# Optimization experiments

Hardware: AMD Instinct MI355X
Metric: run time of the kernel (lower is better)

The kernel has to match this reference:

```python
import jax, jax.numpy as jnp
import numpy as np

DIM = 512
HEADS = 8
DIM_HEAD = 64
INNER = HEADS * DIM_HEAD          # 512
GROUPS = 8                        # offset_groups
OFF_D = INNER // GROUPS           # 64
DS = 4                            # downsample_factor
KS = 6                            # offset_kernel_size
OFF_SCALE = 4.0                   # offset_scale (defaults to downsample_factor)
SCALE = DIM_HEAD ** -0.5


def conv1d(x, w, b=None, stride=1, padding=0, groups=1):
    # x: (B, Cin, N), w: (Cout, Cin//groups, K)
    out = jax.lax.conv_general_dilated(
        x, w, (stride,), [(padding, padding)],
        dimension_numbers=('NCH', 'OIH', 'NCH'), feature_group_count=groups)
    if b is not None:
        out = out + b[None, :, None]
    return out


def grid_sample_1d(feats, grid):
    # Faithful to F.grid_sample(mode='bilinear', padding_mode='zeros', align_corners=False)
    # applied along a length-N axis (the 2D workaround's width dim is size 1 -> identity).
    # feats: (B, C, N), grid: (B, M) normalized coords.
    N = feats.shape[-1]
    pos = ((grid + 1.0) * N - 1.0) * 0.5          # unnormalize, align_corners=False
    x0 = jnp.floor(pos)
    w1 = (pos - x0)[:, None, :]                    # fractional weight, (B,1,M)

    def gather(idx):
        valid = ((idx >= 0) & (idx < N))[:, None, :]
        idxc = jnp.clip(idx, 0, N - 1).astype(jnp.int32)
        g = jnp.take_along_axis(feats, idxc[:, None, :], axis=2)  # (B,C,M)
        return g * valid

    return gather(x0) * (1.0 - w1) + gather(x0 + 1.0) * w1


def setup_inputs() -> dict:
    key = jax.random.key(0)
    ks = jax.random.split(key, 10)
    n = 4096
    x = jax.random.normal(ks[0], (1, n, DIM), dtype=jnp.float32)
    prev_x = jax.random.normal(ks[1], (1, n, DIM), dtype=jnp.float32)

    def w(k, shape, fan_in):
        return jax.random.normal(k, shape, dtype=jnp.float32) * (fan_in ** -0.5)

    Wq = w(ks[2], (INNER, 2 * DIM // GROUPS, 1), 2 * DIM // GROUPS)   # grouped 1x1
    Wk = w(ks[3], (INNER, DIM // GROUPS, 1), DIM // GROUPS)
    Wv = w(ks[4], (INNER, DIM // GROUPS, 1), DIM // GROUPS)
    Wo = w(ks[5], (DIM, INNER, 1), INNER)
    bo = jnp.zeros((DIM,), dtype=jnp.float32)
    Woff_dw = w(ks[6], (OFF_D, 1, KS), KS)                             # depthwise
    boff_dw = jnp.zeros((OFF_D,), dtype=jnp.float32)
    Woff_p = w(ks[7], (1, OFF_D, 1), OFF_D)                            # to 1 channel
    return {"x": x, "prev_x": prev_x, "Wq": Wq, "Wk": Wk, "Wv": Wv,
            "Wo": Wo, "bo": bo, "Woff_dw": Woff_dw, "boff_dw": boff_dw,
            "Woff_p": Woff_p}


def reference(x, prev_x, Wq, Wk, Wv, Wo, bo, Woff_dw, boff_dw, Woff_p):
    b = x.shape[0]                    # must be 1 (module's einsum relies on broadcast)
    x_t = jnp.swapaxes(x, 1, 2)       # (b, dim, n)
    px_t = jnp.swapaxes(prev_x, 1, 2)
    n = x_t.shape[-1]

    cq = jnp.concatenate([px_t, x_t], axis=1)          # (b, 2*dim, n)
    q = conv1d(cq, Wq, groups=GROUPS)                  # (b, inner, n)

    # offset network on grouped queries
    gq = q.reshape(b * GROUPS, OFF_D, n)
    h = conv1d(gq, Woff_dw, boff_dw, stride=DS, padding=(KS - DS) // 2, groups=OFF_D)
    h = jax.nn.gelu(h, approximate=False)
    off = conv1d(h, Woff_p)[:, 0, :]                   # (b*g, m)
    off = jnp.tanh(off) * OFF_SCALE
    m = off.shape[-1]                                  # n // DS

    vgrid = jnp.arange(m, dtype=off.dtype) + off       # (b*g, m)
    vgrid = 2.0 * vgrid / max(m - 1, 1) - 1.0          # normalize_grid
    vgrid = jnp.tile(vgrid, (2, 1))                    # (2*b*g, m)

    kv_in = jnp.concatenate([px_t, x_t], axis=0)       # (2b, dim, n)
    gkv = kv_in.reshape(2 * b * GROUPS, OFF_D, n)
    kv = grid_sample_1d(gkv, vgrid)                    # (2bg, off_d, m)
    kv = kv.reshape(2 * b, INNER, m)

    k = conv1d(kv, Wk, groups=GROUPS)                  # (2b, inner, m)
    v = conv1d(kv, Wv, groups=GROUPS)

    qh = (q * SCALE).reshape(b, HEADS, DIM_HEAD, n).transpose(0, 1, 3, 2)   # (b,h,n,d)
    kh = k.reshape(2 * b, HEADS, DIM_HEAD, m).transpose(0, 1, 3, 2)         # (2b,h,m,d)
    vh = v.reshape(2 * b, HEADS, DIM_HEAD, m).transpose(0, 1, 3, 2)

    qh = jnp.broadcast_to(qh, (2 * b,) + qh.shape[1:])  # explicit torch-einsum broadcast
    sim = jnp.einsum('bhid,bhjd->bhij', qh, kh)         # (2b,h,n,m)
    attn = jax.nn.softmax(sim, axis=-1)
    out = jnp.einsum('bhij,bhjd->bhid', attn, vh)       # (2b,h,n,d)

    out = out.transpose(0, 1, 3, 2).reshape(2 * b, INNER, n)
    out = conv1d(out, Wo, bo)                           # (2b, dim, n)
    out = jnp.swapaxes(out, 1, 2)                       # (2b, n, dim)
    out = out.reshape(2, b, n, DIM)
    return out.mean(axis=0)                             # (b, n, dim) -- avg prev/cur streams
```

## Files before the change

### kernel.cpp

```cpp
#include <hip/hip_runtime.h>
#include <math.h>

#define DIMC 512
#define NG 8
#define QSCALE 0.18033688011112042f
#define MSHIFT 7.2134752044448170f

typedef _Float16 half8 __attribute__((ext_vector_type(8)));
typedef __fp16 fp16x2 __attribute__((ext_vector_type(2)));
typedef float f32x4 __attribute__((ext_vector_type(4)));

__device__ __forceinline__ half8 frag_f32(const float* p) {
    float4 a = *(const float4*)p;
    float4 b = *(const float4*)(p + 4);
    union { fp16x2 h2[4]; half8 h8; } u;
    u.h2[0] = __builtin_amdgcn_cvt_pkrtz(a.x, a.y);
    u.h2[1] = __builtin_amdgcn_cvt_pkrtz(a.z, a.w);
    u.h2[2] = __builtin_amdgcn_cvt_pkrtz(b.x, b.y);
    u.h2[3] = __builtin_amdgcn_cvt_pkrtz(b.z, b.w);
    return u.h8;
}

__global__ __launch_bounds__(256, 2) void k_front(
    const float* __restrict__ x, const float* __restrict__ px,
    const float* __restrict__ Wq, const float* __restrict__ Wk,
    const float* __restrict__ Wv, const float* __restrict__ Wo,
    const float* __restrict__ Wdw, const float* __restrict__ bdw,
    const float* __restrict__ Wp, _Float16* __restrict__ qh,
    _Float16* __restrict__ kt16, _Float16* __restrict__ vt16,
    _Float16* __restrict__ Woh, int n, int m)
{
    __shared__ float Os[64*69];
    __shared__ float hl[2][64];
    __shared__ float part[16][16];
    __shared__ int   x0s[16];
    __shared__ float w1s[16];
    __shared__ _Float16 kvs[2][16*72];
    int g  = blockIdx.x & 7;
    int jt = blockIdx.x >> 3;
    int P0 = jt*64, j0 = jt*16;
    int t  = threadIdx.x;
    int lane = t & 63, w = t >> 6;
    int l15 = lane & 15, quad = lane >> 4;
    const float* SRC = (g < 4) ? px : x;
    int cbase = (g & 3) * 128;

    if (blockIdx.x < 128) {
        int idx = blockIdx.x*2048 + t*8;
        float4 a = *(const float4*)&Wo[idx];
        float4 b = *(const float4*)&Wo[idx+4];
        union { fp16x2 h2[4]; uint4 v; } pk;
        pk.h2[0] = __builtin_amdgcn_cvt_pkrtz(a.x, a.y);
        pk.h2[1] = __builtin_amdgcn_cvt_pkrtz(a.z, a.w);
        pk.h2[2] = __builtin_amdgcn_cvt_pkrtz(b.x, b.y);
        pk.h2[3] = __builtin_amdgcn_cvt_pkrtz(b.z, b.w);
        *(uint4*)&Woh[idx] = pk.v;
    }

    if (t < 128) {
        int side = t >> 6, c = t & 63;
        int p = P0 + (side ? 64 : -1);
        float hsum = 0.f;
        if (p >= 0 && p < n) {
            const float* xr = &SRC[(size_t)p*DIMC + cbase];
            const float* wr = &Wq[(size_t)(g*64 + c)*128];
#pragma unroll 8
            for (int k = 0; k < 32; ++k) {
                float4 xv = *(const float4*)&xr[k*4];
                float4 wv = *(const float4*)&wr[k*4];
                hsum += xv.x*wv.x + xv.y*wv.y + xv.z*wv.z + xv.w*wv.w;
            }
        }
        hl[side][c] = hsum;
    }

    half8 af[4];
#pragma unroll
    for (int ks = 0; ks < 4; ++ks)
        af[ks] = frag_f32(&SRC[(size_t)(P0 + w*16 + l15)*DIMC + cbase + ks*32 + quad*8]);
    f32x4 acc[4];
#pragma unroll
    for (int nt = 0; nt < 4; ++nt) acc[nt] = (f32x4){0.f,0.f,0.f,0.f};
#pragma unroll
    for (int ks = 0; ks < 4; ++ks)
#pragma unroll
        for (int nt = 0; nt < 4; ++nt) {
            half8 bf = frag_f32(&Wq[(size_t)(g*64 + nt*16 + l15)*128 + ks*32 + quad*8]);
            acc[nt] = __builtin_amdgcn_mfma_f32_16x16x32_f16(af[ks], bf, acc[nt], 0, 0, 0);
        }
#pragma unroll
    for (int nt = 0; nt < 4; ++nt)
#pragma unroll
        for (int r = 0; r < 4; ++r)
            Os[(w*16 + quad*4 + r)*69 + nt*16 + l15] = acc[nt][r];
    __syncthreads();

    {
        int i = t >> 2, hf = t & 3;
        union { _Float16 h[16]; uint4 v[2]; } pk;
#pragma unroll
        for (int u = 0; u < 16; ++u) pk.h[u] = (_Float16)(Os[i*69 + hf*16 + u] * QSCALE);
        uint4* dst = (uint4*)&qh[((size_t)g*n + P0 + i)*64 + hf*16];
        dst[0] = pk.v[0]; dst[1] = pk.v[1];
    }

    {
        int j = t & 15, cg = t >> 4;
        float acco = 0.f;
#pragma unroll
        for (int cc = 0; cc < 4; ++cc) {
            int c = cg*4 + cc;
            float h = bdw[c];
#pragma unroll
            for (int tt = 0; tt < 6; ++tt) {
                int lp = 4*j + tt - 1;
                float val = (lp < 0) ? hl[0][c] : (lp >= 64 ? hl[1][c] : Os[lp*69 + c]);
                h += Wdw[c*6 + tt] * val;
            }
            float ge = 0.5f * h * (1.0f + erff(h * 0.70710678118654752f));
            acco += Wp[c] * ge;
        }
        part[cg][j] = acco;
    }
    __syncthreads();
    if (t < 16) {
        float off = 0.f;
#pragma unroll
        for (int cg2 = 0; cg2 < 16; ++cg2) off += part[cg2][t];
        off = tanhf(off) * 4.0f;
        int jg = j0 + t;
        float vg  = 2.0f * ((float)jg + off) / (float)(m - 1) - 1.0f;
        float pos = ((vg + 1.0f) * (float)n - 1.0f) * 0.5f;
        float x0  = floorf(pos);
        x0s[t] = (int)x0;
        w1s[t] = pos - x0;
    }
    __syncthreads();

    {
        float a0[4], a1[4], b0[4], b1[4], wg[4];
#pragma unroll
        for (int jj = 0; jj < 4; ++jj) {
            int j = jj*4 + w;
            int ii = x0s[j];
            wg[jj] = w1s[j];
            bool v0 = (ii   >= 0 && ii   < n);
            bool v1 = (ii+1 >= 0 && ii+1 < n);
            a0[jj] = v0 ? px[(size_t)ii*DIMC + g*64 + lane]     : 0.f;
            a1[jj] = v1 ? px[(size_t)(ii+1)*DIMC + g*64 + lane] : 0.f;
            b0[jj] = v0 ? x[(size_t)ii*DIMC + g*64 + lane]      : 0.f;
            b1[jj] = v1 ? x[(size_t)(ii+1)*DIMC + g*64 + lane]  : 0.f;
        }
#pragma unroll
        for (int jj = 0; jj < 4; ++jj) {
            kvs[0][(jj*4 + w)*72 + lane] = (_Float16)(a0[jj]*(1.0f - wg[jj]) + a1[jj]*wg[jj]);
            kvs[1][(jj*4 + w)*72 + lane] = (_Float16)(b0[jj]*(1.0f - wg[jj]) + b1[jj]*wg[jj]);
        }
    }
    __syncthreads();

    half8 bk[2], bv[2];
#pragma unroll
    for (int ks = 0; ks < 2; ++ks) {
        bk[ks] = frag_f32(&Wk[(size_t)(g*64 + w*16 + l15)*64 + ks*32 + quad*8]);
        bv[ks] = frag_f32(&Wv[(size_t)(g*64 + w*16 + l15)*64 + ks*32 + quad*8]);
    }
#pragma unroll
    for (int s = 0; s < 2; ++s) {
        half8 afk[2];
#pragma unroll
        for (int ks = 0; ks < 2; ++ks)
            afk[ks] = *(const half8*)&kvs[s][l15*72 + ks*32 + quad*8];
        f32x4 ack = (f32x4){0.f,0.f,0.f,0.f};
        f32x4 acv = (f32x4){0.f,0.f,0.f,0.f};
#pragma unroll
        for (int ks = 0; ks < 2; ++ks) {
            ack = __builtin_amdgcn_mfma_f32_16x16x32_f16(afk[ks], bk[ks], ack, 0, 0, 0);
            acv = __builtin_amdgcn_mfma_f32_16x16x32_f16(afk[ks], bv[ks], acv, 0, 0, 0);
        }
        size_t hb = (size_t)(s*8 + g);
#pragma unroll
        for (int r = 0; r < 4; ++r)
            kt16[(hb*m + j0 + quad*4 + r)*64 + w*16 + l15] = (_Float16)ack[r];
        union { fp16x2 h2[2]; uint2 v; } pv;
        pv.h2[0] = __builtin_amdgcn_cvt_pkrtz(acv[0], acv[1]);
        pv.h2[1] = __builtin_amdgcn_cvt_pkrtz(acv[2], acv[3]);
        *(uint2*)&vt16[(hb*64 + w*16 + l15)*m + j0 + quad*4] = pv.v;
    }
}

__global__ __launch_bounds__(256, 2) void k_attn(
    const _Float16* __restrict__ qh, const _Float16* __restrict__ kt16,
    const _Float16* __restrict__ vt16, _Float16* __restrict__ aoh, int n, int m)
{
    __shared__ _Float16 Vs[2][64*72];
    __shared__ _Float16 Ps[128*72];
    int nit = n >> 7;
    int it = blockIdx.x % nit;
    int h  = (blockIdx.x / nit) & 7;
    int s  = blockIdx.x / (nit*8);
    int t  = threadIdx.x;
    int lane = t & 63, w = t >> 6;
    int l15 = lane & 15, quad = lane >> 4;
    int i0 = it*128;

    const _Float16* qb = &qh[((size_t)h*n + i0)*64];
    half8 bqv[2][2];
#pragma unroll
    for (int ks = 0; ks < 2; ++ks)
#pragma unroll
        for (int i2 = 0; i2 < 2; ++i2)
            bqv[ks][i2] = *(const half8*)&qb[(w*32 + i2*16 + l15)*64 + ks*32 + quad*8];

    const _Float16* kb = &kt16[(size_t)(s*8+h)*m*64];
    const _Float16* vb = &vt16[(size_t)(s*8+h)*64*m];

    int r0 = t >> 3, oct = t & 7;

    float lsum[2] = {0.f, 0.f};
    f32x4 oaccT[4][2];
#pragma unroll
    for (int dt = 0; dt < 4; ++dt)
#pragma unroll
        for (int i2 = 0; i2 < 2; ++i2) oaccT[dt][i2] = (f32x4){0.f,0.f,0.f,0.f};

    uint4 pv0 = *(const uint4*)&vb[(size_t)r0*m + oct*8];
    uint4 pv1 = *(const uint4*)&vb[(size_t)(r0+32)*m + oct*8];
    *(uint4*)&Vs[0][r0*72 + oct*8]      = pv0;
    *(uint4*)&Vs[0][(r0+32)*72 + oct*8] = pv1;

    int ntile = m >> 6;
    for (int tk = 0; tk < ntile; ++tk) {
        bool pf = (tk + 1 < ntile);
        if (pf) {
            pv0 = *(const uint4*)&vb[(size_t)r0*m + (tk+1)*64 + oct*8];
            pv1 = *(const uint4*)&vb[(size_t)(r0+32)*m + (tk+1)*64 + oct*8];
        }
        half8 aqv[2][4];
#pragma unroll
        for (int ks = 0; ks < 2; ++ks)
#pragma unroll
            for (int jt = 0; jt < 4; ++jt)
                aqv[ks][jt] = *(const half8*)&kb[(size_t)(tk*64 + jt*16 + l15)*64 + ks*32 + quad*8];

        __syncthreads();
        const _Float16* VB = Vs[tk & 1];
        half8 avv[2][4];
#pragma unroll
        for (int ks = 0; ks < 2; ++ks)
#pragma unroll
            for (int dt = 0; dt < 4; ++dt)
                avv[ks][dt] = *(const half8*)&VB[(dt*16 + l15)*72 + ks*32 + quad*8];

        f32x4 accs[4][2];
#pragma unroll
        for (int jt = 0; jt < 4; ++jt)
#pragma unroll
            for (int i2 = 0; i2 < 2; ++i2) accs[jt][i2] = (f32x4){0.f,0.f,0.f,0.f};
        __builtin_amdgcn_s_setprio(1);
#pragma unroll
        for (int ks = 0; ks < 2; ++ks)
#pragma unroll
            for (int jt = 0; jt < 4; ++jt)
#pragma unroll
                for (int i2 = 0; i2 < 2; ++i2)
                    accs[jt][i2] = __builtin_amdgcn_mfma_f32_16x16x32_f16(
                        aqv[ks][jt], bqv[ks][i2], accs[jt][i2], 0, 0, 0);
        __builtin_amdgcn_s_setprio(0);

#pragma unroll
        for (int jt = 0; jt < 4; ++jt)
#pragma unroll
            for (int i2 = 0; i2 < 2; ++i2) {
                f32x4 p;
#pragma unroll
                for (int r = 0; r < 4; ++r) p[r] = __builtin_amdgcn_exp2f(accs[jt][i2][r] - MSHIFT);
                lsum[i2] += (p[0]+p[1]) + (p[2]+p[3]);
                union { fp16x2 h; int i; } c0, c1;
                c0.h = __builtin_amdgcn_cvt_pkrtz(p[0], p[1]);
                c1.h = __builtin_amdgcn_cvt_pkrtz(p[2], p[3]);
                *(int2*)&Ps[(w*32 + i2*16 + l15)*72 + jt*16 + quad*4] = make_int2(c0.i, c1.i);
            }

        __builtin_amdgcn_s_setprio(1);
#pragma unroll
        for (int ks = 0; ks < 2; ++ks)
#pragma unroll
            for (int i2 = 0; i2 < 2; ++i2) {
                half8 bp = *(const half8*)&Ps[(w*32 + i2*16 + l15)*72 + ks*32 + quad*8];
#pragma unroll
                for (int dt = 0; dt < 4; ++dt)
                    oaccT[dt][i2] = __builtin_amdgcn_mfma_f32_16x16x32_f16(
                        avv[ks][dt], bp, oaccT[dt][i2], 0, 0, 0);
            }
        __builtin_amdgcn_s_setprio(0);

        if (pf) {
            int b2 = (tk + 1) & 1;
            *(uint4*)&Vs[b2][r0*72 + oct*8]      = pv0;
            *(uint4*)&Vs[b2][(r0+32)*72 + oct*8] = pv1;
        }
    }

#pragma unroll
    for (int i2 = 0; i2 < 2; ++i2) {
        lsum[i2] += __shfl_xor(lsum[i2], 16, 64);
        lsum[i2] += __shfl_xor(lsum[i2], 32, 64);
    }
    float inv[2] = {1.0f / lsum[0], 1.0f / lsum[1]};
#pragma unroll
    for (int dt = 0; dt < 4; ++dt)
#pragma unroll
        for (int i2 = 0; i2 < 2; ++i2)
#pragma unroll
            for (int r = 0; r < 4; ++r)
                Ps[(w*32 + i2*16 + l15)*72 + dt*16 + quad*4 + r]
                    = (_Float16)(oaccT[dt][i2][r] * inv[i2]);
    {
        int row = w*32 + (lane >> 1);
        int dbase = (lane & 1) * 32;
        size_t gbase = (size_t)(i0 + row)*1024 + s*512 + h*64 + dbase;
#pragma unroll
        for (int k2 = 0; k2 < 4; ++k2) {
            uint4 v = *(uint4*)&Ps[row*72 + dbase + k2*8];
            *(uint4*)&aoh[gbase + k2*8] = v;
        }
    }
}

__global__ __launch_bounds__(256) void k_out(
    const _Float16* __restrict__ aoh, const _Float16* __restrict__ Woh,
    const float* __restrict__ bo, float* __restrict__ out, int n)
{
    int i0 = blockIdx.x*64, d0 = blockIdx.y*64;
    int t = threadIdx.x;
    int lane = t & 63, w = t >> 6;
    int l15 = lane & 15, quad = lane >> 4;
    f32x4 oacc[4];
#pragma unroll
    for (int dt = 0; dt < 4; ++dt) oacc[dt] = (f32x4){0.f,0.f,0.f,0.f};

    const _Float16* arow = &aoh[(size_t)(i0 + w*16 + l15)*1024 + quad*8];
#pragma unroll 4
    for (int ks = 0; ks < 16; ++ks) {
        half8 aq0 = *(const half8*)&arow[ks*32];
        half8 aq1 = *(const half8*)&arow[(ks+16)*32];
        int cbase = ks * 32;
#pragma unroll
        for (int dt = 0; dt < 4; ++dt) {
            half8 bw = *(const half8*)&Woh[(size_t)(d0 + dt*16 + l15)*DIMC + cbase + quad*8];
            oacc[dt] = __builtin_amdgcn_mfma_f32_16x16x32_f16(aq0, bw, oacc[dt], 0, 0, 0);
            oacc[dt] = __builtin_amdgcn_mfma_f32_16x16x32_f16(aq1, bw, oacc[dt], 0, 0, 0);
        }
    }
#pragma unroll
    for (int dt = 0; dt < 4; ++dt) {
        float bias = bo[d0 + dt*16 + l15];
#pragma unroll
        for (int r = 0; r < 4; ++r)
            out[(size_t)(i0 + w*16 + quad*4 + r)*DIMC + d0 + dt*16 + l15]
                = bias + 0.5f*oacc[dt][r];
    }
}

extern "C" void kernel_launch(void* const* d_in, const int* in_sizes, int n_in,
                              void* d_out, int out_size, void* d_ws, size_t ws_size,
                              hipStream_t stream)
{
    const float* x   = (const float*)d_in[0];
    const float* px  = (const float*)d_in[1];
    const float* Wq  = (const float*)d_in[2];
    const float* Wk  = (const float*)d_in[3];
    const float* Wv  = (const float*)d_in[4];
    const float* Wo  = (const float*)d_in[5];
    const float* bo  = (const float*)d_in[6];
    const float* Wdw = (const float*)d_in[7];
    const float* bdw = (const float*)d_in[8];
    const float* Wp  = (const float*)d_in[9];
    float* out = (float*)d_out;
    int n = in_sizes[0] / DIMC;
    int m = n / 4;

    _Float16* qhf  = (_Float16*)d_ws;
    _Float16* kt16 = qhf + (size_t)8*n*64;
    _Float16* vt16 = kt16 + (size_t)16*m*64;
    _Float16* aoh  = vt16 + (size_t)16*m*64;
    _Float16* Woh  = aoh + (size_t)n*1024;

    k_front<<<8*(m/16),    256, 0, stream>>>(x, px, Wq, Wk, Wv, Wo, Wdw, bdw, Wp,
                                             qhf, kt16, vt16, Woh, n, m);
    k_attn <<<2*8*(n/128), 256, 0, stream>>>(qhf, kt16, vt16, aoh, n, m);
    k_out  <<<dim3(n/64, 8), 256, 0, stream>>>(aoh, Woh, bo, out, n);
}
```

Measured before the change: 158.6 us.

## Halve per-block tiles in front and output-projection kernels to double block count

```diff
diff --git a/kernel.cpp b/kernel.cpp
--- a/kernel.cpp
+++ b/kernel.cpp
@@ -21,7 +21,7 @@
     return u.h8;
 }
 
-__global__ __launch_bounds__(256, 2) void k_front(
+__global__ __launch_bounds__(256, 4) void k_front(
     const float* __restrict__ x, const float* __restrict__ px,
     const float* __restrict__ Wq, const float* __restrict__ Wk,
     const float* __restrict__ Wv, const float* __restrict__ Wo,
@@ -30,15 +30,15 @@
     _Float16* __restrict__ kt16, _Float16* __restrict__ vt16,
     _Float16* __restrict__ Woh, int n, int m)
 {
-    __shared__ float Os[64*69];
+    __shared__ float Os[32*69];
     __shared__ float hl[2][64];
-    __shared__ float part[16][16];
-    __shared__ int   x0s[16];
-    __shared__ float w1s[16];
-    __shared__ _Float16 kvs[2][16*72];
+    __shared__ float part[32][8];
+    __shared__ int   x0s[8];
+    __shared__ float w1s[8];
+    __shared__ _Float16 kvs[2][8*72];
     int g  = blockIdx.x & 7;
     int jt = blockIdx.x >> 3;
-    int P0 = jt*64, j0 = jt*16;
+    int P0 = jt*32, j0 = jt*8;
     int t  = threadIdx.x;
     int lane = t & 63, w = t >> 6;
     int l15 = lane & 15, quad = lane >> 4;
@@ -59,7 +59,7 @@
 
     if (t < 128) {
         int side = t >> 6, c = t & 63;
-        int p = P0 + (side ? 64 : -1);
+        int p = P0 + (side ? 32 : -1);
         float hsum = 0.f;
         if (p >= 0 && p < n) {
             const float* xr = &SRC[(size_t)p*DIMC + cbase];
@@ -74,47 +74,48 @@
         hl[side][c] = hsum;
     }
 
-    half8 af[4];
-#pragma unroll
-    for (int ks = 0; ks < 4; ++ks)
-        af[ks] = frag_f32(&SRC[(size_t)(P0 + w*16 + l15)*DIMC + cbase + ks*32 + quad*8]);
-    f32x4 acc[4];
-#pragma unroll
-    for (int nt = 0; nt < 4; ++nt) acc[nt] = (f32x4){0.f,0.f,0.f,0.f};
-#pragma unroll
-    for (int ks = 0; ks < 4; ++ks)
-#pragma unroll
-        for (int nt = 0; nt < 4; ++nt) {
-            half8 bf = frag_f32(&Wq[(size_t)(g*64 + nt*16 + l15)*128 + ks*32 + quad*8]);
-            acc[nt] = __builtin_amdgcn_mfma_f32_16x16x32_f16(af[ks], bf, acc[nt], 0, 0, 0);
-        }
-#pragma unroll
-    for (int nt = 0; nt < 4; ++nt)
+    half8 af[2][4];
+#pragma unroll
+    for (int mt = 0; mt < 2; ++mt)
+#pragma unroll
+        for (int ks = 0; ks < 4; ++ks)
+            af[mt][ks] = frag_f32(&SRC[(size_t)(P0 + mt*16 + l15)*DIMC + cbase + ks*32 + quad*8]);
+    f32x4 acc[2];
+#pragma unroll
+    for (int mt = 0; mt < 2; ++mt) acc[mt] = (f32x4){0.f,0.f,0.f,0.f};
+#pragma unroll
+    for (int ks = 0; ks < 4; ++ks) {
+        half8 bf = frag_f32(&Wq[(size_t)(g*64 + w*16 + l15)*128 + ks*32 + quad*8]);
+#pragma unroll
+        for (int mt = 0; mt < 2; ++mt)
+            acc[mt] = __builtin_amdgcn_mfma_f32_16x16x32_f16(af[mt][ks], bf, acc[mt], 0, 0, 0);
+    }
+#pragma unroll
+    for (int mt = 0; mt < 2; ++mt)
 #pragma unroll
         for (int r = 0; r < 4; ++r)
-            Os[(w*16 + quad*4 + r)*69 + nt*16 + l15] = acc[nt][r];
+            Os[(mt*16 + quad*4 + r)*69 + w*16 + l15] = acc[mt][r];
     __syncthreads();
 
     {
-        int i = t >> 2, hf = t & 3;
-        union { _Float16 h[16]; uint4 v[2]; } pk;
-#pragma unroll
-        for (int u = 0; u < 16; ++u) pk.h[u] = (_Float16)(Os[i*69 + hf*16 + u] * QSCALE);
-        uint4* dst = (uint4*)&qh[((size_t)g*n + P0 + i)*64 + hf*16];
-        dst[0] = pk.v[0]; dst[1] = pk.v[1];
+        int i = t >> 3, hf = t & 7;
+        union { _Float16 h[8]; uint4 v; } pk;
+#pragma unroll
+        for (int u = 0; u < 8; ++u) pk.h[u] = (_Float16)(Os[i*69 + hf*8 + u] * QSCALE);
+        *(uint4*)&qh[((size_t)g*n + P0 + i)*64 + hf*8] = pk.v;
     }
 
     {
-        int j = t & 15, cg = t >> 4;
+        int j = t & 7, cg = t >> 3;
         float acco = 0.f;
 #pragma unroll
-        for (int cc = 0; cc < 4; ++cc) {
-            int c = cg*4 + cc;
+        for (int cc = 0; cc < 2; ++cc) {
+            int c = cg*2 + cc;
             float h = bdw[c];
 #pragma unroll
             for (int tt = 0; tt < 6; ++tt) {
                 int lp = 4*j + tt - 1;
-                float val = (lp < 0) ? hl[0][c] : (lp >= 64 ? hl[1][c] : Os[lp*69 + c]);
+                float val = (lp < 0) ? hl[0][c] : (lp >= 32 ? hl[1][c] : Os[lp*69 + c]);
                 h += Wdw[c*6 + tt] * val;
             }
             float ge = 0.5f * h * (1.0f + erff(h * 0.70710678118654752f));
@@ -123,10 +124,10 @@
         part[cg][j] = acco;
     }
     __syncthreads();
-    if (t < 16) {
+    if (t < 8) {
         float off = 0.f;
 #pragma unroll
-        for (int cg2 = 0; cg2 < 16; ++cg2) off += part[cg2][t];
+        for (int cg2 = 0; cg2 < 32; ++cg2) off += part[cg2][t];
         off = tanhf(off) * 4.0f;
         int jg = j0 + t;
         float vg  = 2.0f * ((float)jg + off) / (float)(m - 1) - 1.0f;
@@ -138,10 +139,10 @@
     __syncthreads();
 
     {
-        float a0[4], a1[4], b0[4], b1[4], wg[4];
-#pragma unroll
-        for (int jj = 0; jj < 4; ++jj) {
-            int j = jj*4 + w;
+        float a0[2], a1[2], b0[2], b1[2], wg[2];
+#pragma unroll
+        for (int jj = 0; jj < 2; ++jj) {
+            int j = w*2 + jj;
             int ii = x0s[j];
             wg[jj] = w1s[j];
             bool v0 = (ii   >= 0 && ii   < n);
@@ -152,9 +153,9 @@
             b1[jj] = v1 ? x[(size_t)(ii+1)*DIMC + g*64 + lane]  : 0.f;
         }
 #pragma unroll
-        for (int jj = 0; jj < 4; ++jj) {
-            kvs[0][(jj*4 + w)*72 + lane] = (_Float16)(a0[jj]*(1.0f - wg[jj]) + a1[jj]*wg[jj]);
-            kvs[1][(jj*4 + w)*72 + lane] = (_Float16)(b0[jj]*(1.0f - wg[jj]) + b1[jj]*wg[jj]);
+        for (int jj = 0; jj < 2; ++jj) {
+            kvs[0][(w*2 + jj)*72 + lane] = (_Float16)(a0[jj]*(1.0f - wg[jj]) + a1[jj]*wg[jj]);
+            kvs[1][(w*2 + jj)*72 + lane] = (_Float16)(b0[jj]*(1.0f - wg[jj]) + b1[jj]*wg[jj]);
         }
     }
     __syncthreads();
@@ -165,12 +166,15 @@
         bk[ks] = frag_f32(&Wk[(size_t)(g*64 + w*16 + l15)*64 + ks*32 + quad*8]);
         bv[ks] = frag_f32(&Wv[(size_t)(g*64 + w*16 + l15)*64 + ks*32 + quad*8]);
     }
+    half8 zf;
+#pragma unroll
+    for (int u = 0; u < 8; ++u) zf[u] = (_Float16)0.f;
 #pragma unroll
     for (int s = 0; s < 2; ++s) {
         half8 afk[2];
 #pragma unroll
         for (int ks = 0; ks < 2; ++ks)
-            afk[ks] = *(const half8*)&kvs[s][l15*72 + ks*32 + quad*8];
+            afk[ks] = (l15 < 8) ? *(const half8*)&kvs[s][l15*72 + ks*32 + quad*8] : zf;
         f32x4 ack = (f32x4){0.f,0.f,0.f,0.f};
         f32x4 acv = (f32x4){0.f,0.f,0.f,0.f};
 #pragma unroll
@@ -179,13 +183,15 @@
             acv = __builtin_amdgcn_mfma_f32_16x16x32_f16(afk[ks], bv[ks], acv, 0, 0, 0);
         }
         size_t hb = (size_t)(s*8 + g);
-#pragma unroll
-        for (int r = 0; r < 4; ++r)
-            kt16[(hb*m + j0 + quad*4 + r)*64 + w*16 + l15] = (_Float16)ack[r];
-        union { fp16x2 h2[2]; uint2 v; } pv;
-        pv.h2[0] = __builtin_amdgcn_cvt_pkrtz(acv[0], acv[1]);
-        pv.h2[1] = __builtin_amdgcn_cvt_pkrtz(acv[2], acv[3]);
-        *(uint2*)&vt16[(hb*64 + w*16 + l15)*m + j0 + quad*4] = pv.v;
+        if (quad < 2) {
+#pragma unroll
+            for (int r = 0; r < 4; ++r)
+                kt16[(hb*m + j0 + quad*4 + r)*64 + w*16 + l15] = (_Float16)ack[r];
+            union { fp16x2 h2[2]; uint2 v; } pv;
+            pv.h2[0] = __builtin_amdgcn_cvt_pkrtz(acv[0], acv[1]);
+            pv.h2[1] = __builtin_amdgcn_cvt_pkrtz(acv[2], acv[3]);
+            *(uint2*)&vt16[(hb*64 + w*16 + l15)*m + j0 + quad*4] = pv.v;
+        }
     }
 }
 
@@ -328,37 +334,38 @@
     }
 }
 
-__global__ __launch_bounds__(256) void k_out(
+__global__ __launch_bounds__(256, 4) void k_out(
     const _Float16* __restrict__ aoh, const _Float16* __restrict__ Woh,
     const float* __restrict__ bo, float* __restrict__ out, int n)
 {
-    int i0 = blockIdx.x*64, d0 = blockIdx.y*64;
+    int i0 = blockIdx.x*32, d0 = blockIdx.y*64;
     int t = threadIdx.x;
     int lane = t & 63, w = t >> 6;
     int l15 = lane & 15, quad = lane >> 4;
-    f32x4 oacc[4];
-#pragma unroll
-    for (int dt = 0; dt < 4; ++dt) oacc[dt] = (f32x4){0.f,0.f,0.f,0.f};
-
-    const _Float16* arow = &aoh[(size_t)(i0 + w*16 + l15)*1024 + quad*8];
+    int wi = w & 1, wd = w >> 1;
+    f32x4 oacc[2];
+#pragma unroll
+    for (int dt = 0; dt < 2; ++dt) oacc[dt] = (f32x4){0.f,0.f,0.f,0.f};
+
+    const _Float16* arow = &aoh[(size_t)(i0 + wi*16 + l15)*1024 + quad*8];
 #pragma unroll 4
     for (int ks = 0; ks < 16; ++ks) {
         half8 aq0 = *(const half8*)&arow[ks*32];
         half8 aq1 = *(const half8*)&arow[(ks+16)*32];
         int cbase = ks * 32;
 #pragma unroll
-        for (int dt = 0; dt < 4; ++dt) {
-            half8 bw = *(const half8*)&Woh[(size_t)(d0 + dt*16 + l15)*DIMC + cbase + quad*8];
+        for (int dt = 0; dt < 2; ++dt) {
+            half8 bw = *(const half8*)&Woh[(size_t)(d0 + wd*32 + dt*16 + l15)*DIMC + cbase + quad*8];
             oacc[dt] = __builtin_amdgcn_mfma_f32_16x16x32_f16(aq0, bw, oacc[dt], 0, 0, 0);
             oacc[dt] = __builtin_amdgcn_mfma_f32_16x16x32_f16(aq1, bw, oacc[dt], 0, 0, 0);
         }
     }
 #pragma unroll
-    for (int dt = 0; dt < 4; ++dt) {
-        float bias = bo[d0 + dt*16 + l15];
+    for (int dt = 0; dt < 2; ++dt) {
+        float bias = bo[d0 + wd*32 + dt*16 + l15];
 #pragma unroll
         for (int r = 0; r < 4; ++r)
-            out[(size_t)(i0 + w*16 + quad*4 + r)*DIMC + d0 + dt*16 + l15]
+            out[(size_t)(i0 + wi*16 + quad*4 + r)*DIMC + d0 + wd*32 + dt*16 + l15]
                 = bias + 0.5f*oacc[dt][r];
     }
 }
@@ -387,8 +394,8 @@
     _Float16* aoh  = vt16 + (size_t)16*m*64;
     _Float16* Woh  = aoh + (size_t)n*1024;
 
-    k_front<<<8*(m/16),    256, 0, stream>>>(x, px, Wq, Wk, Wv, Wo, Wdw, bdw, Wp,
+    k_front<<<8*(m/8),     256, 0, stream>>>(x, px, Wq, Wk, Wv, Wo, Wdw, bdw, Wp,
                                              qhf, kt16, vt16, Woh, n, m);
     k_attn <<<2*8*(n/128), 256, 0, stream>>>(qhf, kt16, vt16, aoh, n, m);
-    k_out  <<<dim3(n/64, 8), 256, 0, stream>>>(aoh, Woh, bo, out, n);
+    k_out  <<<dim3(n/32, 8), 256, 0, stream>>>(aoh, Woh, bo, out, n);
 }
```

Result: slower. 172.9 us (+9.0%).
